# Kernel optimization log

Measured on AMD Instinct MI355X. Metric: run time of the kernel, lower is better.

Reference implementation:

```python
import jax, jax.numpy as jnp
import numpy as np
import math

B, DIM, H, W = 16, 384, 64, 64
SCALES, HEADS, HID = 4, 4, 32
WIDTH = DIM // SCALES
NUMS = SCALES - 1
PH = PW = 2
LS = 1e-6


def setup_inputs():
    ks = jax.random.split(jax.random.key(0), 20)
    n = lambda i, shape, s=0.02: jax.random.normal(ks[i], shape, jnp.float32) * s
    return {
        'x': jax.random.normal(ks[0], (B, DIM, H, W), jnp.float32),
        'convs_w': n(1, (NUMS, WIDTH, 3, 3)), 'convs_b': n(2, (NUMS, WIDTH)),
        'pos_w': n(3, (DIM, 2 * HID)), 'pos_b': n(4, (DIM,)),
        'ln_xca_w': jnp.ones((DIM,), jnp.float32), 'ln_xca_b': jnp.zeros((DIM,), jnp.float32),
        'gamma_xca': jnp.full((DIM,), LS, jnp.float32),
        'xca_temp': jnp.ones((HEADS, 1, 1), jnp.float32),
        'xca_kv_w': n(5, (2 * DIM, DIM)), 'xca_kv_b': n(6, (2 * DIM,)),
        'xca_proj_w': n(7, (DIM, DIM)), 'xca_proj_b': n(8, (DIM,)),
        'conv_out_w': n(9, (DIM,)), 'conv_out_b': n(10, (DIM,)),
        'wa_kv_w': n(11, (2 * DIM, DIM)), 'wa_kv_b': n(12, (2 * DIM,)),
        'wa_proj_w': n(13, (DIM, DIM)), 'wa_proj_b': n(14, (DIM,)),
        'ln_w': jnp.ones((DIM,), jnp.float32), 'ln_b': jnp.zeros((DIM,), jnp.float32),
        'pw1_w': n(15, (4 * DIM, DIM)), 'pw1_b': n(16, (4 * DIM,)),
        'pw2_w': n(17, (DIM, 4 * DIM)), 'pw2_b': n(18, (DIM,)),
        'gamma': jnp.full((DIM,), LS, jnp.float32),
    }


def layer_norm(x, w, b, eps=1e-6):
    m = jnp.mean(x, -1, keepdims=True)
    v = jnp.mean((x - m) ** 2, -1, keepdims=True)
    return (x - m) * jax.lax.rsqrt(v + eps) * w + b


def l2norm(x, eps=1e-12):  # torch F.normalize over last dim
    return x / jnp.maximum(jnp.linalg.norm(x, axis=-1, keepdims=True), eps)


def dwconv3x3(x, w, b):  # depthwise: w [Cw,3,3]
    out = jax.lax.conv_general_dilated(x, w[:, None], (1, 1), ((1, 1), (1, 1)),
        dimension_numbers=('NCHW', 'OIHW', 'NCHW'), feature_group_count=w.shape[0])
    return out + b[None, :, None, None]


def pos_fourier(pos_w, pos_b):  # -> [H*W, DIM] (batch-independent since mask is all-false)
    scale = 2 * math.pi
    y = jnp.arange(1, H + 1, dtype=jnp.float32)[:, None] / (H + 1e-6) * scale
    xg = jnp.arange(1, W + 1, dtype=jnp.float32)[None, :] / (W + 1e-6) * scale
    y = jnp.broadcast_to(y, (H, W))
    xg = jnp.broadcast_to(xg, (H, W))
    dim_t = jnp.arange(HID, dtype=jnp.float32)
    dim_t = 10000.0 ** (2 * jnp.floor(dim_t / 2) / HID)
    px = xg[..., None] / dim_t
    py = y[..., None] / dim_t
    px = jnp.stack((jnp.sin(px[..., 0::2]), jnp.cos(px[..., 1::2])), -1).reshape(H, W, HID)
    py = jnp.stack((jnp.sin(py[..., 0::2]), jnp.cos(py[..., 1::2])), -1).reshape(H, W, HID)
    pos = jnp.concatenate((py, px), -1)  # [H,W,2*HID]
    return (pos @ pos_w.T + pos_b).reshape(H * W, DIM)


def xca_fn(x, const, kv_w, kv_b, proj_w, proj_b, temp):
    b, n, c = x.shape
    h, hd = HEADS, c // HEADS
    q1 = const.reshape(b, n, h, hd).transpose(0, 2, 3, 1)          # b,h,hd,n
    kv = (x @ kv_w.T + kv_b).reshape(b, n, 2, h, hd).transpose(2, 0, 3, 1, 4)
    k = l2norm(kv[0].transpose(0, 1, 3, 2))                        # b,h,hd,n (L2 over n)
    v = kv[1].transpose(0, 1, 3, 2)                                # b,h,hd,n
    attn = jax.nn.softmax(jnp.einsum('bhcn,bhdn->bhcd', q1, k) * temp, -1)
    out = jnp.einsum('bhcd,bhdn->bhcn', attn, v)
    out = out.transpose(0, 3, 1, 2).reshape(b, n, c)
    return out @ proj_w.T + proj_b


def window_attn(x, const, kv_w, kv_b, proj_w, proj_b):
    b, n, c = x.shape
    h, hd = HEADS, c // HEADS
    kv = (x @ kv_w.T + kv_b).reshape(b, n, 2, h, hd).transpose(2, 0, 3, 1, 4)
    k = l2norm(kv[0].transpose(0, 1, 3, 2))                        # b,h,hd,n
    v = kv[1].transpose(0, 1, 3, 2)                                # b,h,hd,n
    q1 = const.reshape(b, n, 1, h, hd).transpose(2, 0, 3, 1, 4)    # 1,b,h,n,hd (leading 1 kept, as in torch)
    q1 = q1.transpose(0, 1, 2, 4, 3)                               # 1,b,h,hd,n
    logits = jnp.einsum('obhcn,bhdn->obhcd', q1, k)
    attn = 0.5 * logits / math.sqrt(hd) + 0.5 * jax.nn.softmax(logits, -1)
    attn = jax.nn.softmax(attn, -1)
    out = jnp.einsum('obhcd,bhdn->obhcn', attn, v)                 # 1,b,h,hd,n
    out = out.transpose(0, 2, 1, 3, 4).reshape(b, n, c)            # torch .transpose(1,2).reshape(B,N,C)
    return out @ proj_w.T + proj_b


def unfold(x):  # H,W divisible by patch -> no interpolate branch
    b, c = x.shape[0], x.shape[1]
    nph, npw = H // PH, W // PW
    x = x.reshape(b * c * nph, PH, npw, PW).transpose(0, 2, 1, 3)
    x = x.reshape(b, c, nph * npw, PH * PW).transpose(0, 3, 2, 1)
    return x.reshape(b * PH * PW, nph * npw, c)


def fold(x):
    c = x.shape[-1]
    nph, npw = H // PH, W // PW
    x = x.reshape(B, PH * PW, nph * npw, c).transpose(0, 3, 2, 1)
    x = x.reshape(B * c * nph, npw, PH, PW).transpose(0, 2, 1, 3)
    return x.reshape(B, c, nph * PH, npw * PW)


def reference(x, convs_w, convs_b, pos_w, pos_b, ln_xca_w, ln_xca_b, gamma_xca,
              xca_temp, xca_kv_w, xca_kv_b, xca_proj_w, xca_proj_b,
              conv_out_w, conv_out_b, wa_kv_w, wa_kv_b, wa_proj_w, wa_proj_b,
              ln_w, ln_b, pw1_w, pw1_b, pw2_w, pw2_b, gamma):
    inp = x
    # multi-scale depthwise convs (Res2Net style)
    spx = jnp.split(x, SCALES, axis=1)
    outs = []
    sp = spx[0]
    for i in range(NUMS):
        if i > 0:
            sp = sp + spx[i]
        sp = dwconv3x3(sp, convs_w[i], convs_b[i])
        outs.append(sp)
    x = jnp.concatenate(outs + [spx[NUMS]], axis=1)
    N = H * W
    x3 = x.reshape(B, DIM, N).transpose(0, 2, 1)                   # B,N,C
    x3 = x3 + pos_fourier(pos_w, pos_b)[None]
    const = inp.reshape(B, DIM, N).transpose(0, 2, 1)
    x4 = x3 + gamma_xca * xca_fn(layer_norm(x3, ln_xca_w, ln_xca_b), const,
                                 xca_kv_w, xca_kv_b, xca_proj_w, xca_proj_b, xca_temp)
    x4 = x4.reshape(B, H, W, DIM).transpose(0, 3, 1, 2)
    # conv_out: Conv2d(dim,dim,1,groups=dim) == per-channel scale+bias
    x = x4 * conv_out_w[None, :, None, None] + conv_out_b[None, :, None, None]
    x2 = window_attn(unfold(x), unfold(inp), wa_kv_w, wa_kv_b, wa_proj_w, wa_proj_b)
    x = fold(x2).transpose(0, 2, 3, 1)                             # B,H,W,C
    x = layer_norm(x, ln_w, ln_b)
    x = jax.nn.gelu(x @ pw1_w.T + pw1_b, approximate=False)
    x = x @ pw2_w.T + pw2_b
    x = gamma * x
    return inp + x.transpose(0, 3, 1, 2)
```

## Files before the change

### kernel.cpp

```cpp
#include <hip/hip_runtime.h>
#include <math.h>

#define NBATCH 16
#define CDIM   384
#define NPIX   4096
#define HDCH   96
#define NROWS  65536
#define KVHALF 25165824

typedef unsigned short bf16;
typedef __attribute__((ext_vector_type(8))) short short8;
typedef __attribute__((ext_vector_type(4))) float floatx4;

union S8U { short8 v; bf16 u[8]; };

__device__ __forceinline__ float b2f(bf16 u) {
    union { unsigned int i; float f; } c; c.i = ((unsigned int)u) << 16; return c.f;
}
__device__ __forceinline__ bf16 f2b(float f) {
    union { float f; unsigned int i; } c; c.f = f;
    unsigned int r = (c.i + 0x7FFFu + ((c.i >> 16) & 1u)) >> 16;
    return (bf16)r;
}

__global__ __launch_bounds__(256) void zero_kernel(float* __restrict__ p) {
    p[blockIdx.x * 256 + threadIdx.x] = 0.0f;
}

__global__ __launch_bounds__(128) void pos_kernel(const float* __restrict__ pos_w,
                                                  const float* __restrict__ pos_b,
                                                  bf16* __restrict__ pos) {
    __shared__ float feat[64];
    int n = blockIdx.x;
    int yi = n >> 6, xi = n & 63;
    int tid = threadIdx.x;
    if (tid < 64) {
        int j = tid & 31;
        int isx = tid >= 32;
        float base = (float)((isx ? xi : yi) + 1);
        float val = base / (64.0f + 1e-6f) * 6.283185307179586f;
        float e = (float)(2 * (j >> 1)) / 32.0f;
        float dt = powf(10000.0f, e);
        float a = val / dt;
        feat[isx * 32 + j] = (j & 1) ? cosf(a) : sinf(a);
    }
    __syncthreads();
    for (int c = tid; c < CDIM; c += 128) {
        float s = pos_b[c];
        const float* wr = pos_w + c * 64;
        #pragma unroll 16
        for (int j = 0; j < 64; ++j) s += feat[j] * wr[j];
        pos[n * CDIM + c] = f2b(s);
    }
}

__global__ __launch_bounds__(256) void dwconv_kernel(const float* __restrict__ xin, int in_ch0,
                                                     const bf16* __restrict__ prev, int prev_ch0,
                                                     const float* __restrict__ w,
                                                     const float* __restrict__ bias,
                                                     bf16* __restrict__ out, int out_ch0) {
    __shared__ float tile[66][66];
    int b = blockIdx.x / 96, c = blockIdx.x % 96;
    const float* ip = xin + (b * CDIM + in_ch0 + c) * NPIX;
    const bf16* pp = prev ? prev + (b * CDIM + prev_ch0 + c) * NPIX : nullptr;
    int tid = threadIdx.x;
    for (int i = tid; i < 66 * 66; i += 256) {
        int yy = i / 66 - 1, xx = i % 66 - 1;
        float v = 0.0f;
        if (yy >= 0 && yy < 64 && xx >= 0 && xx < 64) {
            v = ip[yy * 64 + xx];
            if (pp) v += b2f(pp[yy * 64 + xx]);
        }
        tile[i / 66][i % 66] = v;
    }
    __syncthreads();
    float wc[9];
    #pragma unroll
    for (int j = 0; j < 9; ++j) wc[j] = w[c * 9 + j];
    float b0 = bias[c];
    bf16* op = out + (b * CDIM + out_ch0 + c) * NPIX;
    for (int p = tid; p < NPIX; p += 256) {
        int y = p >> 6, x = p & 63;
        float a = b0;
        #pragma unroll
        for (int dy = 0; dy < 3; ++dy)
            #pragma unroll
            for (int dx = 0; dx < 3; ++dx)
                a += tile[y + dy][x + dx] * wc[dy * 3 + dx];
        op[p] = f2b(a);
    }
}

__global__ __launch_bounds__(256) void convert_last_kernel(const float* __restrict__ x,
                                                           bf16* __restrict__ xcat) {
    int idx = blockIdx.x * 256 + threadIdx.x;
    int b = idx / (96 * 1024);
    int rem = idx % (96 * 1024);
    const float4* src = (const float4*)(x + (b * CDIM + 288) * NPIX);
    float4 v = src[rem];
    ushort4 o;
    o.x = f2b(v.x); o.y = f2b(v.y); o.z = f2b(v.z); o.w = f2b(v.w);
    ((ushort4*)(xcat + (b * CDIM + 288) * NPIX))[rem] = o;
}

__global__ void x3_kernel(const bf16* __restrict__ xcat, const bf16* __restrict__ pos,
                          bf16* __restrict__ x3) {
    __shared__ float t[32][33];
    int c0 = blockIdx.x * 32, n0 = blockIdx.y * 32, b = blockIdx.z;
    int tx = threadIdx.x, ty = threadIdx.y;
    #pragma unroll
    for (int k = 0; k < 4; ++k) {
        int cl = ty + k * 8;
        t[cl][tx] = b2f(xcat[(b * CDIM + c0 + cl) * NPIX + n0 + tx]);
    }
    __syncthreads();
    #pragma unroll
    for (int k = 0; k < 4; ++k) {
        int nl = ty + k * 8;
        x3[(b * NPIX + n0 + nl) * CDIM + c0 + tx] =
            f2b(t[tx][nl] + b2f(pos[(n0 + nl) * CDIM + c0 + tx]));
    }
}

__global__ __launch_bounds__(128) void ln_kernel(const bf16* __restrict__ in,
                                                 const float* __restrict__ w,
                                                 const float* __restrict__ b,
                                                 bf16* __restrict__ out, int map) {
    int r = blockIdx.x;
    int src = r;
    if (map == 1) {
        int bb = r >> 12;
        int p = r & 4095;
        int y = p >> 6, x = p & 63;
        int patch = ((y & 1) << 1) | (x & 1);
        int blk = ((y >> 1) << 5) | (x >> 1);
        src = ((bb << 2) + patch) * 1024 + blk;
    }
    const bf16* row = in + src * CDIM;
    int tid = threadIdx.x;
    float v[3];
    float s1 = 0.0f, s2 = 0.0f;
    #pragma unroll
    for (int i = 0; i < 3; ++i) {
        v[i] = b2f(row[tid + i * 128]);
        s1 += v[i];
        s2 += v[i] * v[i];
    }
    __shared__ float r1[128], r2[128];
    r1[tid] = s1; r2[tid] = s2;
    __syncthreads();
    for (int off = 64; off > 0; off >>= 1) {
        if (tid < off) { r1[tid] += r1[tid + off]; r2[tid] += r2[tid + off]; }
        __syncthreads();
    }
    float mean = r1[0] * (1.0f / 384.0f);
    float var = fmaxf(r2[0] * (1.0f / 384.0f) - mean * mean, 0.0f);
    float rstd = rsqrtf(var + 1e-6f);
    #pragma unroll
    for (int i = 0; i < 3; ++i) {
        int c = tid + i * 128;
        out[r * CDIM + c] = f2b((v[i] - mean) * rstd * w[c] + b[c]);
    }
}

#define LDP 48
__global__ __launch_bounds__(256) void mfma_gemm_kernel(const bf16* __restrict__ A,
                                                        const float* __restrict__ W,
                                                        const float* __restrict__ bias,
                                                        bf16* __restrict__ C,
                                                        int M, int Nout, int K, int mode,
                                                        const bf16* __restrict__ res,
                                                        const float* __restrict__ scalevec,
                                                        int nlog2) {
    __shared__ bf16 As[128][LDP];
    __shared__ bf16 Bs[128][LDP];
    int m0 = blockIdx.x * 128;
    int n0 = blockIdx.y * 128;
    int tid = threadIdx.x;
    int wave = tid >> 6, lane = tid & 63;
    int wm = (wave & 1) * 64;
    int wn = (wave >> 1) * 64;
    int quad = lane >> 4;
    int lrow = lane & 15;

    int sRow = tid >> 1;
    int sK = (tid & 1) * 16;

    floatx4 acc[4][4] = {};

    for (int k0 = 0; k0 < K; k0 += 32) {
        const bf16* ap = A + (size_t)(m0 + sRow) * K + k0 + sK;
        short8 a0 = *(const short8*)(ap);
        short8 a1 = *(const short8*)(ap + 8);
        const float* wp = W + (size_t)(n0 + sRow) * K + k0 + sK;
        float4 w0 = *(const float4*)(wp);
        float4 w1 = *(const float4*)(wp + 4);
        float4 w2 = *(const float4*)(wp + 8);
        float4 w3 = *(const float4*)(wp + 12);
        union { short8 v; bf16 u[8]; } p0, p1;
        p0.u[0] = f2b(w0.x); p0.u[1] = f2b(w0.y); p0.u[2] = f2b(w0.z); p0.u[3] = f2b(w0.w);
        p0.u[4] = f2b(w1.x); p0.u[5] = f2b(w1.y); p0.u[6] = f2b(w1.z); p0.u[7] = f2b(w1.w);
        p1.u[0] = f2b(w2.x); p1.u[1] = f2b(w2.y); p1.u[2] = f2b(w2.z); p1.u[3] = f2b(w2.w);
        p1.u[4] = f2b(w3.x); p1.u[5] = f2b(w3.y); p1.u[6] = f2b(w3.z); p1.u[7] = f2b(w3.w);
        __syncthreads();
        *(short8*)(&As[sRow][sK])     = a0;
        *(short8*)(&As[sRow][sK + 8]) = a1;
        *(short8*)(&Bs[sRow][sK])     = p0.v;
        *(short8*)(&Bs[sRow][sK + 8]) = p1.v;
        __syncthreads();
        short8 af[4], bfr[4];
        #pragma unroll
        for (int i = 0; i < 4; ++i)
            af[i] = *(const short8*)(&As[wm + i * 16 + lrow][quad * 8]);
        #pragma unroll
        for (int j = 0; j < 4; ++j)
            bfr[j] = *(const short8*)(&Bs[wn + j * 16 + lrow][quad * 8]);
        #pragma unroll
        for (int i = 0; i < 4; ++i)
            #pragma unroll
            for (int j = 0; j < 4; ++j)
                acc[i][j] = __builtin_amdgcn_mfma_f32_16x16x32_bf16(af[i], bfr[j], acc[i][j], 0, 0, 0);
    }

    if (mode == 3) {
        int nmask = (1 << nlog2) - 1;
        #pragma unroll
        for (int i = 0; i < 4; ++i) {
            int rowb = m0 + wm + i * 16 + quad * 4;
            int bb = rowb >> nlog2, tok = rowb & nmask;
            #pragma unroll
            for (int j = 0; j < 4; ++j) {
                int col = n0 + wn + j * 16 + lrow;
                float bv = bias[col];
                if (col < 384) {
                    ushort4 o;
                    o.x = f2b(acc[i][j][0] + bv);
                    o.y = f2b(acc[i][j][1] + bv);
                    o.z = f2b(acc[i][j][2] + bv);
                    o.w = f2b(acc[i][j][3] + bv);
                    *(ushort4*)(C + ((((size_t)bb * 384 + col) << nlog2) | (size_t)tok)) = o;
                } else {
                    bf16* vp = C + KVHALF + (size_t)rowb * 384 + (col - 384);
                    #pragma unroll
                    for (int r = 0; r < 4; ++r)
                        vp[(size_t)r * 384] = f2b(acc[i][j][r] + bv);
                }
            }
        }
        return;
    }

    #pragma unroll
    for (int i = 0; i < 4; ++i) {
        int rowb = m0 + wm + i * 16 + quad * 4;
        #pragma unroll
        for (int j = 0; j < 4; ++j) {
            int col = n0 + wn + j * 16 + lrow;
            float bv = bias[col];
            #pragma unroll
            for (int r = 0; r < 4; ++r) {
                int row = rowb + r;
                float v = acc[i][j][r] + bv;
                if (mode == 1) {
                    v = 0.5f * v * (1.0f + erff(v * 0.70710678118654752f));
                } else if (mode == 2) {
                    v = b2f(res[(size_t)row * Nout + col]) + scalevec[col] * v;
                }
                C[(size_t)row * Nout + col] = f2b(v);
            }
        }
    }
}

__global__ __launch_bounds__(256) void knormsq2_kernel(const bf16* __restrict__ KT,
                                                       float* __restrict__ outk, int n_len) {
    int row = blockIdx.x;
    const bf16* p = KT + (size_t)row * n_len;
    int tid = threadIdx.x;
    float s = 0.0f;
    for (int i = tid * 8; i < n_len; i += 256 * 8) {
        S8U t; t.v = *(const short8*)(p + i);
        #pragma unroll
        for (int j = 0; j < 8; ++j) { float f = b2f(t.u[j]); s += f * f; }
    }
    __shared__ float red[256];
    red[tid] = s;
    __syncthreads();
    for (int off = 128; off > 0; off >>= 1) {
        if (tid < off) red[tid] += red[tid + off];
        __syncthreads();
    }
    if (tid == 0) outk[row] = red[0];
}

__global__ __launch_bounds__(256) void chan_qk_mfma(const float* __restrict__ qf,
                                                    const bf16* __restrict__ qb,
                                                    const bf16* __restrict__ KT,
                                                    float* __restrict__ Sg,
                                                    int n_len, int nchunks, int mode) {
    int pair = blockIdx.x / nchunks, ck = blockIdx.x % nchunks;
    int bi = pair >> 2, h = pair & 3;
    int koff = h * HDCH;
    int chunk = n_len / nchunks;
    int nbeg = ck * chunk;
    int tid = threadIdx.x;
    int wave = tid >> 6, lane = tid & 63;
    int lr = lane & 15, q = lane >> 4;
    int c0 = (wave & 1) * 48;
    int d0 = (wave >> 1) * 48;
    floatx4 acc[3][3] = {};
    const size_t qbase = (size_t)(bi * CDIM + koff) * n_len;
    const bf16* kbase = KT + (size_t)(bi * CDIM + koff) * n_len;
    for (int nn = 0; nn < chunk; nn += 32) {
        int n0 = nbeg + nn + q * 8;
        short8 af[3], bfr[3];
        if (mode == 0) {
            #pragma unroll
            for (int i = 0; i < 3; ++i) {
                const float* qp = qf + qbase + (size_t)(c0 + i * 16 + lr) * n_len + n0;
                float4 f0 = *(const float4*)qp;
                float4 f1 = *(const float4*)(qp + 4);
                S8U t;
                t.u[0] = f2b(f0.x); t.u[1] = f2b(f0.y); t.u[2] = f2b(f0.z); t.u[3] = f2b(f0.w);
                t.u[4] = f2b(f1.x); t.u[5] = f2b(f1.y); t.u[6] = f2b(f1.z); t.u[7] = f2b(f1.w);
                af[i] = t.v;
            }
        } else {
            #pragma unroll
            for (int i = 0; i < 3; ++i)
                af[i] = *(const short8*)(qb + qbase + (size_t)(c0 + i * 16 + lr) * n_len + n0);
        }
        #pragma unroll
        for (int j = 0; j < 3; ++j)
            bfr[j] = *(const short8*)(kbase + (size_t)(d0 + j * 16 + lr) * n_len + n0);
        #pragma unroll
        for (int i = 0; i < 3; ++i)
            #pragma unroll
            for (int j = 0; j < 3; ++j)
                acc[i][j] = __builtin_amdgcn_mfma_f32_16x16x32_bf16(af[i], bfr[j], acc[i][j], 0, 0, 0);
    }
    float* Sp = Sg + (size_t)pair * 9216;
    #pragma unroll
    for (int i = 0; i < 3; ++i) {
        int rowb = c0 + i * 16 + q * 4;
        #pragma unroll
        for (int j = 0; j < 3; ++j) {
            int col = d0 + j * 16 + lr;
            #pragma unroll
            for (int r = 0; r < 4; ++r)
                atomicAdd(&Sp[(rowb + r) * 96 + col], acc[i][j][r]);
        }
    }
}

__global__ __launch_bounds__(128) void chan_softmax_kernel(const float* __restrict__ Sg,
                                                           const float* __restrict__ knsq,
                                                           const float* __restrict__ temp,
                                                           bf16* __restrict__ Sb,
                                                           int mode) {
    __shared__ float knrm[96];
    int pair = blockIdx.x;
    int bi = pair >> 2, h = pair & 3;
    int tid = threadIdx.x;
    if (tid < 96)
        knrm[tid] = 1.0f / fmaxf(sqrtf(knsq[bi * CDIM + h * HDCH + tid]), 1e-12f);
    __syncthreads();
    if (tid >= 96) return;
    const float* Sr = Sg + (size_t)pair * 9216 + tid * 96;
    bf16* Ob = Sb + (size_t)pair * 9216 + tid * 96;
    if (mode == 0) {
        float tv = temp[h];
        float m = -1e30f;
        for (int d = 0; d < 96; ++d) m = fmaxf(m, Sr[d] * knrm[d] * tv);
        float s = 0.0f;
        for (int d = 0; d < 96; ++d) s += expf(Sr[d] * knrm[d] * tv - m);
        float inv = 1.0f / s;
        for (int d = 0; d < 96; ++d) Ob[d] = f2b(expf(Sr[d] * knrm[d] * tv - m) * inv);
    } else {
        const float RSQ = 0.10206207261596575f;
        float m1 = -1e30f;
        for (int d = 0; d < 96; ++d) m1 = fmaxf(m1, Sr[d] * knrm[d]);
        float s1 = 0.0f;
        for (int d = 0; d < 96; ++d) s1 += expf(Sr[d] * knrm[d] - m1);
        float inv1 = 1.0f / s1;
        float m2 = -1e30f;
        for (int d = 0; d < 96; ++d) {
            float l = Sr[d] * knrm[d];
            float a = 0.5f * l * RSQ + 0.5f * expf(l - m1) * inv1;
            m2 = fmaxf(m2, a);
        }
        float s2 = 0.0f;
        for (int d = 0; d < 96; ++d) {
            float l = Sr[d] * knrm[d];
            float a = 0.5f * l * RSQ + 0.5f * expf(l - m1) * inv1;
            s2 += expf(a - m2);
        }
        float inv2 = 1.0f / s2;
        for (int d = 0; d < 96; ++d) {
            float l = Sr[d] * knrm[d];
            float a = 0.5f * l * RSQ + 0.5f * expf(l - m1) * inv1;
            Ob[d] = f2b(expf(a - m2) * inv2);
        }
    }
}

#define PVTN 256
__global__ __launch_bounds__(256) void chan_pv_mfma(const bf16* __restrict__ Sb,
                                                    const bf16* __restrict__ V,
                                                    bf16* __restrict__ out,
                                                    int n_len, int mode) {
    int nch = n_len / PVTN;
    int pair = blockIdx.x / nch, ck = blockIdx.x % nch;
    int bi = pair >> 2, h = pair & 3;
    int koff = h * HDCH;
    int tid = threadIdx.x;
    int wave = tid >> 6, lane = tid & 63;
    int lr = lane & 15, q = lane >> 4;
    const bf16* Ab = Sb + (size_t)pair * 9216;
    short8 af[6][3];
    #pragma unroll
    for (int i = 0; i < 6; ++i)
        #pragma unroll
        for (int kt = 0; kt < 3; ++kt)
            af[i][kt] = *(const short8*)(Ab + (i * 16 + lr) * 96 + kt * 32 + q * 8);
    const bf16* vb = V + (size_t)bi * n_len * 384 + koff;
    int nbase = ck * PVTN + wave * 16;
    #pragma unroll
    for (int s = 0; s < 4; ++s) {
        int n = nbase + s * 64 + lr;
        short8 bfr[3];
        #pragma unroll
        for (int kt = 0; kt < 3; ++kt)
            bfr[kt] = *(const short8*)(vb + (size_t)n * 384 + kt * 32 + q * 8);
        floatx4 acc[6] = {};
        #pragma unroll
        for (int kt = 0; kt < 3; ++kt)
            #pragma unroll
            for (int i = 0; i < 6; ++i)
                acc[i] = __builtin_amdgcn_mfma_f32_16x16x32_bf16(af[i][kt], bfr[kt], acc[i], 0, 0, 0);
        if (mode == 0) {
            bf16* op = out + (size_t)(bi * n_len + n) * CDIM + koff;
            #pragma unroll
            for (int i = 0; i < 6; ++i) {
                ushort4 o;
                o.x = f2b(acc[i][0]); o.y = f2b(acc[i][1]);
                o.z = f2b(acc[i][2]); o.w = f2b(acc[i][3]);
                *(ushort4*)(op + i * 16 + q * 4) = o;
            }
        } else {
            #pragma unroll
            for (int i = 0; i < 6; ++i) {
                int cb = i * 16 + q * 4;
                #pragma unroll
                for (int r = 0; r < 4; ++r)
                    out[(size_t)((h * 64 + bi) * HDCH + cb + r) * n_len + n] = f2b(acc[i][r]);
            }
        }
    }
}

__global__ __launch_bounds__(256) void unfold_cu_kernel(const float* __restrict__ xin,
                                                        bf16* __restrict__ cu) {
    int idx = blockIdx.x * 256 + threadIdx.x;
    int b2 = idx / (CDIM * 1024);
    int rem = idx % (CDIM * 1024);
    int ch = rem >> 10, blk = rem & 1023;
    int b = b2 >> 2, patch = b2 & 3;
    int y = ((blk >> 5) << 1) | (patch >> 1);
    int x = ((blk & 31) << 1) | (patch & 1);
    cu[idx] = f2b(xin[(size_t)(b * CDIM + ch) * NPIX + (y << 6) + x]);
}

__global__ __launch_bounds__(256) void unfold_xu_kernel(const bf16* __restrict__ x4,
                                                        const float* __restrict__ cw,
                                                        const float* __restrict__ cb,
                                                        bf16* __restrict__ xu) {
    int idx = blockIdx.x * 256 + threadIdx.x;
    int row = idx / CDIM, ch = idx % CDIM;
    int b2 = row >> 10, blk = row & 1023;
    int b = b2 >> 2, patch = b2 & 3;
    int y = ((blk >> 5) << 1) | (patch >> 1);
    int x = ((blk & 31) << 1) | (patch & 1);
    xu[idx] = f2b(b2f(x4[(size_t)(b * NPIX + (y << 6) + x) * CDIM + ch]) * cw[ch] + cb[ch]);
}

__global__ void out_kernel(const float* __restrict__ xin, const bf16* __restrict__ fin,
                           const float* __restrict__ gamma, float* __restrict__ outp) {
    __shared__ float t[32][33];
    int c0 = blockIdx.x * 32, p0 = blockIdx.y * 32, b = blockIdx.z;
    int tx = threadIdx.x, ty = threadIdx.y;
    #pragma unroll
    for (int k = 0; k < 4; ++k) {
        int pl = ty + k * 8;
        t[pl][tx] = b2f(fin[(size_t)(b * NPIX + p0 + pl) * CDIM + c0 + tx]);
    }
    __syncthreads();
    #pragma unroll
    for (int k = 0; k < 4; ++k) {
        int cl = ty + k * 8;
        size_t addr = (size_t)(b * CDIM + c0 + cl) * NPIX + p0 + tx;
        outp[addr] = xin[addr] + gamma[c0 + cl] * t[tx][cl];
    }
}

extern "C" void kernel_launch(void* const* d_in, const int* in_sizes, int n_in,
                              void* d_out, int out_size, void* d_ws, size_t ws_size,
                              hipStream_t stream) {
    (void)in_sizes; (void)n_in; (void)out_size; (void)ws_size;
    const float* x         = (const float*)d_in[0];
    const float* convs_w   = (const float*)d_in[1];
    const float* convs_b   = (const float*)d_in[2];
    const float* pos_w     = (const float*)d_in[3];
    const float* pos_b     = (const float*)d_in[4];
    const float* ln_xca_w  = (const float*)d_in[5];
    const float* ln_xca_b  = (const float*)d_in[6];
    const float* gamma_xca = (const float*)d_in[7];
    const float* xca_temp  = (const float*)d_in[8];
    const float* xca_kv_w  = (const float*)d_in[9];
    const float* xca_kv_b  = (const float*)d_in[10];
    const float* xca_proj_w= (const float*)d_in[11];
    const float* xca_proj_b= (const float*)d_in[12];
    const float* conv_out_w= (const float*)d_in[13];
    const float* conv_out_b= (const float*)d_in[14];
    const float* wa_kv_w   = (const float*)d_in[15];
    const float* wa_kv_b   = (const float*)d_in[16];
    const float* wa_proj_w = (const float*)d_in[17];
    const float* wa_proj_b = (const float*)d_in[18];
    const float* ln_w      = (const float*)d_in[19];
    const float* ln_b      = (const float*)d_in[20];
    const float* pw1_w     = (const float*)d_in[21];
    const float* pw1_b     = (const float*)d_in[22];
    const float* pw2_w     = (const float*)d_in[23];
    const float* pw2_b     = (const float*)d_in[24];
    const float* gamma     = (const float*)d_in[25];
    float* out = (float*)d_out;

    bf16* pos = (bf16*)d_ws;
    bf16* P1  = pos + 1572864;
    bf16* P2  = P1 + 25165824;
    bf16* P3  = P2 + 25165824;
    float* knsq    = (float*)(P3 + 50331648);
    float* knsq_wa = knsq + 6144;
    float* S_xca   = knsq_wa + 24576;
    float* S_wa    = S_xca + 589824;

    zero_kernel<<<11640, 256, 0, stream>>>(knsq);

    pos_kernel<<<4096, 128, 0, stream>>>(pos_w, pos_b, pos);

    dwconv_kernel<<<NBATCH * 96, 256, 0, stream>>>(x,   0, nullptr, 0,  convs_w,        convs_b,       P1, 0);
    dwconv_kernel<<<NBATCH * 96, 256, 0, stream>>>(x,  96, P1,      0,  convs_w + 864,  convs_b + 96,  P1, 96);
    dwconv_kernel<<<NBATCH * 96, 256, 0, stream>>>(x, 192, P1,     96,  convs_w + 1728, convs_b + 192, P1, 192);
    convert_last_kernel<<<6144, 256, 0, stream>>>(x, P1);

    x3_kernel<<<dim3(12, 128, NBATCH), dim3(32, 8), 0, stream>>>(P1, pos, P2);

    ln_kernel<<<NROWS, 128, 0, stream>>>(P2, ln_xca_w, ln_xca_b, P1, 0);
    mfma_gemm_kernel<<<dim3(512, 6), 256, 0, stream>>>(P1, xca_kv_w, xca_kv_b, P3,
                                                       NROWS, 768, 384, 3, nullptr, nullptr, 12);
    knormsq2_kernel<<<6144, 256, 0, stream>>>(P3, knsq, 4096);
    chan_qk_mfma<<<512, 256, 0, stream>>>(x, nullptr, P3, S_xca, 4096, 8, 0);
    chan_softmax_kernel<<<64, 128, 0, stream>>>(S_xca, knsq, xca_temp, pos, 0);
    chan_pv_mfma<<<1024, 256, 0, stream>>>(pos, P3 + KVHALF, P1, 4096, 0);
    mfma_gemm_kernel<<<dim3(512, 3), 256, 0, stream>>>(P1, xca_proj_w, xca_proj_b, P3,
                                                       NROWS, 384, 384, 2, P2, gamma_xca, 0);

    unfold_cu_kernel<<<98304, 256, 0, stream>>>(x, P2);
    unfold_xu_kernel<<<98304, 256, 0, stream>>>(P3, conv_out_w, conv_out_b, P1);
    mfma_gemm_kernel<<<dim3(512, 6), 256, 0, stream>>>(P1, wa_kv_w, wa_kv_b, P3,
                                                       NROWS, 768, 384, 3, nullptr, nullptr, 10);
    knormsq2_kernel<<<24576, 256, 0, stream>>>(P3, knsq_wa, 1024);
    chan_qk_mfma<<<512, 256, 0, stream>>>(nullptr, P2, P3, S_wa, 1024, 2, 1);
    chan_softmax_kernel<<<256, 128, 0, stream>>>(S_wa, knsq_wa, nullptr, P2, 1);
    chan_pv_mfma<<<1024, 256, 0, stream>>>(P2, P3 + KVHALF, P1, 1024, 1);
    mfma_gemm_kernel<<<dim3(512, 3), 256, 0, stream>>>(P1, wa_proj_w, wa_proj_b, P2,
                                                       NROWS, 384, 384, 0, nullptr, nullptr, 0);

    ln_kernel<<<NROWS, 128, 0, stream>>>(P2, ln_w, ln_b, P1, 1);
    for (int ch = 0; ch < 4; ++ch) {
        mfma_gemm_kernel<<<dim3(128, 12), 256, 0, stream>>>(P1 + (size_t)ch * 16384 * 384, pw1_w, pw1_b,
                                                            P3, 16384, 1536, 384, 1, nullptr, nullptr, 0);
        mfma_gemm_kernel<<<dim3(128, 3), 256, 0, stream>>>(P3, pw2_w, pw2_b,
                                                           P2 + (size_t)ch * 16384 * 384, 16384, 384, 1536,
                                                           0, nullptr, nullptr, 0);
    }

    out_kernel<<<dim3(12, 128, NBATCH), dim3(32, 8), 0, stream>>>(x, P2, gamma, out);
}
```

Measured before the change: 1.536 ms.

## Pre-convert GEMM weights to bf16 and stage tiles via direct global-to-LDS loads

Adds a small kernel that converts each fp32 weight matrix to bf16 once before its GEMM, so the GEMM no longer loads fp32 weights and converts them per tile. The GEMM now stages A and B tiles with global_load_lds (direct global-to-LDS) using an XOR-swizzled unpadded layout to avoid bank conflicts on fragment reads. This cuts weight bandwidth and VALU work and removes register staging. In exchange it adds extra launches and reuses the pos buffer region as scratch for the weights, which is only safe if pos is dead by then.

```diff
diff --git a/kernel.cpp b/kernel.cpp
--- a/kernel.cpp
+++ b/kernel.cpp
@@ -23,8 +23,25 @@
     return (bf16)r;
 }
 
+__device__ __forceinline__ void gload16(const bf16* g, bf16* l) {
+    __builtin_amdgcn_global_load_lds(
+        (const __attribute__((address_space(1))) unsigned int*)g,
+        (__attribute__((address_space(3))) unsigned int*)l, 16, 0, 0);
+}
+
 __global__ __launch_bounds__(256) void zero_kernel(float* __restrict__ p) {
     p[blockIdx.x * 256 + threadIdx.x] = 0.0f;
+}
+
+__global__ __launch_bounds__(256) void wcvt_kernel(const float* __restrict__ w,
+                                                   bf16* __restrict__ o, int n4) {
+    int i = blockIdx.x * 256 + threadIdx.x;
+    if (i < n4) {
+        float4 v = ((const float4*)w)[i];
+        ushort4 u;
+        u.x = f2b(v.x); u.y = f2b(v.y); u.z = f2b(v.z); u.w = f2b(v.w);
+        ((ushort4*)o)[i] = u;
+    }
 }
 
 __global__ __launch_bounds__(128) void pos_kernel(const float* __restrict__ pos_w,
@@ -163,17 +180,16 @@
     }
 }
 
-#define LDP 48
 __global__ __launch_bounds__(256) void mfma_gemm_kernel(const bf16* __restrict__ A,
-                                                        const float* __restrict__ W,
+                                                        const bf16* __restrict__ W,
                                                         const float* __restrict__ bias,
                                                         bf16* __restrict__ C,
                                                         int M, int Nout, int K, int mode,
                                                         const bf16* __restrict__ res,
                                                         const float* __restrict__ scalevec,
                                                         int nlog2) {
-    __shared__ bf16 As[128][LDP];
-    __shared__ bf16 Bs[128][LDP];
+    __shared__ bf16 As[128][32];
+    __shared__ bf16 Bs[128][32];
     int m0 = blockIdx.x * 128;
     int n0 = blockIdx.y * 128;
     int tid = threadIdx.x;
@@ -183,38 +199,38 @@
     int quad = lane >> 4;
     int lrow = lane & 15;
 
-    int sRow = tid >> 1;
-    int sK = (tid & 1) * 16;
+    int p0b = wave * 1024 + lane * 16;
+    int o0 = p0b ^ (((p0b >> 7) & 3) << 4);
+    int r0 = o0 >> 6;
+    int ch0 = (o0 >> 4) & 3;
+
+    const bf16* aSrc0 = A + (size_t)(m0 + r0) * K + ch0 * 8;
+    const bf16* aSrc1 = A + (size_t)(m0 + r0 + 64) * K + ch0 * 8;
+    const bf16* bSrc0 = W + (size_t)(n0 + r0) * K + ch0 * 8;
+    const bf16* bSrc1 = W + (size_t)(n0 + r0 + 64) * K + ch0 * 8;
+    bf16* lA0 = &As[0][0] + wave * 512;
+    bf16* lA1 = &As[0][0] + 2048 + wave * 512;
+    bf16* lB0 = &Bs[0][0] + wave * 512;
+    bf16* lB1 = &Bs[0][0] + 2048 + wave * 512;
+
+    int rcol = (quad ^ ((lrow >> 1) & 3)) * 8;
 
     floatx4 acc[4][4] = {};
 
     for (int k0 = 0; k0 < K; k0 += 32) {
-        const bf16* ap = A + (size_t)(m0 + sRow) * K + k0 + sK;
-        short8 a0 = *(const short8*)(ap);
-        short8 a1 = *(const short8*)(ap + 8);
-        const float* wp = W + (size_t)(n0 + sRow) * K + k0 + sK;
-        float4 w0 = *(const float4*)(wp);
-        float4 w1 = *(const float4*)(wp + 4);
-        float4 w2 = *(const float4*)(wp + 8);
-        float4 w3 = *(const float4*)(wp + 12);
-        union { short8 v; bf16 u[8]; } p0, p1;
-        p0.u[0] = f2b(w0.x); p0.u[1] = f2b(w0.y); p0.u[2] = f2b(w0.z); p0.u[3] = f2b(w0.w);
-        p0.u[4] = f2b(w1.x); p0.u[5] = f2b(w1.y); p0.u[6] = f2b(w1.z); p0.u[7] = f2b(w1.w);
-        p1.u[0] = f2b(w2.x); p1.u[1] = f2b(w2.y); p1.u[2] = f2b(w2.z); p1.u[3] = f2b(w2.w);
-        p1.u[4] = f2b(w3.x); p1.u[5] = f2b(w3.y); p1.u[6] = f2b(w3.z); p1.u[7] = f2b(w3.w);
         __syncthreads();
-        *(short8*)(&As[sRow][sK])     = a0;
-        *(short8*)(&As[sRow][sK + 8]) = a1;
-        *(short8*)(&Bs[sRow][sK])     = p0.v;
-        *(short8*)(&Bs[sRow][sK + 8]) = p1.v;
+        gload16(aSrc0 + k0, lA0);
+        gload16(aSrc1 + k0, lA1);
+        gload16(bSrc0 + k0, lB0);
+        gload16(bSrc1 + k0, lB1);
         __syncthreads();
         short8 af[4], bfr[4];
         #pragma unroll
         for (int i = 0; i < 4; ++i)
-            af[i] = *(const short8*)(&As[wm + i * 16 + lrow][quad * 8]);
+            af[i] = *(const short8*)(&As[wm + i * 16 + lrow][rcol]);
         #pragma unroll
         for (int j = 0; j < 4; ++j)
-            bfr[j] = *(const short8*)(&Bs[wn + j * 16 + lrow][quad * 8]);
+            bfr[j] = *(const short8*)(&Bs[wn + j * 16 + lrow][rcol]);
         #pragma unroll
         for (int i = 0; i < 4; ++i)
             #pragma unroll
@@ -544,6 +560,9 @@
     float* S_xca   = knsq_wa + 24576;
     float* S_wa    = S_xca + 589824;
 
+    bf16* wbufA = pos + 589824;
+    bf16* wbufB = pos;
+
     zero_kernel<<<11640, 256, 0, stream>>>(knsq);
 
     pos_kernel<<<4096, 128, 0, stream>>>(pos_w, pos_b, pos);
@@ -556,31 +575,37 @@
     x3_kernel<<<dim3(12, 128, NBATCH), dim3(32, 8), 0, stream>>>(P1, pos, P2);
 
     ln_kernel<<<NROWS, 128, 0, stream>>>(P2, ln_xca_w, ln_xca_b, P1, 0);
-    mfma_gemm_kernel<<<dim3(512, 6), 256, 0, stream>>>(P1, xca_kv_w, xca_kv_b, P3,
+    wcvt_kernel<<<288, 256, 0, stream>>>(xca_kv_w, wbufA, 73728);
+    mfma_gemm_kernel<<<dim3(512, 6), 256, 0, stream>>>(P1, wbufA, xca_kv_b, P3,
                                                        NROWS, 768, 384, 3, nullptr, nullptr, 12);
     knormsq2_kernel<<<6144, 256, 0, stream>>>(P3, knsq, 4096);
     chan_qk_mfma<<<512, 256, 0, stream>>>(x, nullptr, P3, S_xca, 4096, 8, 0);
     chan_softmax_kernel<<<64, 128, 0, stream>>>(S_xca, knsq, xca_temp, pos, 0);
     chan_pv_mfma<<<1024, 256, 0, stream>>>(pos, P3 + KVHALF, P1, 4096, 0);
-    mfma_gemm_kernel<<<dim3(512, 3), 256, 0, stream>>>(P1, xca_proj_w, xca_proj_b, P3,
+    wcvt_kernel<<<144, 256, 0, stream>>>(xca_proj_w, wbufA, 36864);
+    mfma_gemm_kernel<<<dim3(512, 3), 256, 0, stream>>>(P1, wbufA, xca_proj_b, P3,
                                                        NROWS, 384, 384, 2, P2, gamma_xca, 0);
 
     unfold_cu_kernel<<<98304, 256, 0, stream>>>(x, P2);
     unfold_xu_kernel<<<98304, 256, 0, stream>>>(P3, conv_out_w, conv_out_b, P1);
-    mfma_gemm_kernel<<<dim3(512, 6), 256, 0, stream>>>(P1, wa_kv_w, wa_kv_b, P3,
+    wcvt_kernel<<<288, 256, 0, stream>>>(wa_kv_w, wbufA, 73728);
+    mfma_gemm_kernel<<<dim3(512, 6), 256, 0, stream>>>(P1, wbufA, wa_kv_b, P3,
                                                        NROWS, 768, 384, 3, nullptr, nullptr, 10);
     knormsq2_kernel<<<24576, 256, 0, stream>>>(P3, knsq_wa, 1024);
     chan_qk_mfma<<<512, 256, 0, stream>>>(nullptr, P2, P3, S_wa, 1024, 2, 1);
     chan_softmax_kernel<<<256, 128, 0, stream>>>(S_wa, knsq_wa, nullptr, P2, 1);
     chan_pv_mfma<<<1024, 256, 0, stream>>>(P2, P3 + KVHALF, P1, 1024, 1);
-    mfma_gemm_kernel<<<dim3(512, 3), 256, 0, stream>>>(P1, wa_proj_w, wa_proj_b, P2,
+    wcvt_kernel<<<144, 256, 0, stream>>>(wa_proj_w, wbufA, 36864);
+    mfma_gemm_kernel<<<dim3(512, 3), 256, 0, stream>>>(P1, wbufA, wa_proj_b, P2,
                                                        NROWS, 384, 384, 0, nullptr, nullptr, 0);
 
     ln_kernel<<<NROWS, 128, 0, stream>>>(P2, ln_w, ln_b, P1, 1);
+    wcvt_kernel<<<576, 256, 0, stream>>>(pw1_w, wbufA, 147456);
+    wcvt_kernel<<<576, 256, 0, stream>>>(pw2_w, wbufB, 147456);
     for (int ch = 0; ch < 4; ++ch) {
-        mfma_gemm_kernel<<<dim3(128, 12), 256, 0, stream>>>(P1 + (size_t)ch * 16384 * 384, pw1_w, pw1_b,
+        mfma_gemm_kernel<<<dim3(128, 12), 256, 0, stream>>>(P1 + (size_t)ch * 16384 * 384, wbufA, pw1_b,
                                                             P3, 16384, 1536, 384, 1, nullptr, nullptr, 0);
-        mfma_gemm_kernel<<<dim3(128, 3), 256, 0, stream>>>(P3, pw2_w, pw2_b,
+        mfma_gemm_kernel<<<dim3(128, 3), 256, 0, stream>>>(P3, wbufB, pw2_b,
                                                            P2 + (size_t)ch * 16384 * 384, 16384, 384, 1536,
                                                            0, nullptr, nullptr, 0);
     }
```

Measured after the change: 1.360 ms. 11.4% less time.
